# Kernel tuning notes

Measured on AMD Instinct MI355X. Metric: run time of the kernel, lower is better.

## Reference

```python
import jax, jax.numpy as jnp
import numpy as np

EPS = 1e-3        # Memory.eps distance threshold
MOMENTUM = 0.999  # Memory.momentum
N, F, M = 500000, 256, 1024


def setup_inputs() -> dict:
    key = jax.random.key(0)
    k1, k2, k3, k4, k5 = jax.random.split(key, 5)
    return {
        "points": jax.random.normal(k1, (M, 3), dtype=jnp.float32),
        "descriptors": jax.random.normal(k2, (M, F), dtype=jnp.float32),
        # learned/stateful memory bank (params/buffers of the module)
        "mem_points": jax.random.normal(k3, (N, 3), dtype=jnp.float32),
        "mem_descriptors": jax.random.normal(k4, (N, F), dtype=jnp.float32),
        "usage": jax.random.randint(k5, (N,), 0, 1000, dtype=jnp.int32),
    }


def _moving(x, m):
    # faithful to Memory.moving: x*m + (1-m)*x  (== x, kept as written)
    return x * m + (1.0 - m) * x


def reference(points, descriptors, mem_points, mem_descriptors, usage):
    # ---- point_address: cdist (p=2) + argmin nearest neighbor ----
    # squared-distance expansion; [M, N] matrix
    d2 = (jnp.sum(points * points, axis=-1)[:, None]
          + jnp.sum(mem_points * mem_points, axis=-1)[None, :]
          - 2.0 * points @ mem_points.T)
    dist = jnp.sqrt(jnp.maximum(d2, 1e-12))
    dmin = jnp.min(dist, axis=-1)
    idx = jnp.argmin(dist, axis=-1)            # [M]
    mask = dmin > EPS                          # queries with no near match

    # ---- topk eviction: lowest-usage slots, assigned in query order ----
    # torch: idx[mask] = usage.topk(k=mask.sum(), largest=False).indices
    # static-shape equivalent: take top-M least-used, select first cumsum(mask)
    _, evict = jax.lax.top_k(-usage, points.shape[0])  # [M] least-used slots
    rank = jnp.cumsum(mask.astype(jnp.int32)) - 1      # position among masked
    idx = jnp.where(mask, evict[rank], idx)

    momentum = jnp.where(mask, 0.0, MOMENTUM)[:, None]  # [M, 1]

    # ---- write: usage bump + momentum scatter-update ----
    usage_new = usage.at[idx].add(1)
    pts_new = mem_points.at[idx].set(_moving(mem_points[idx], momentum))
    desc_new = mem_descriptors.at[idx].set(_moving(mem_descriptors[idx], momentum))

    out = jnp.concatenate([pts_new, desc_new], axis=1)  # [N, 3+F]
    return out, usage_new, idx
```

## Files before the change

### kernel.cpp

```cpp
#include <hip/hip_runtime.h>

#define N_TOT   500000
#define M_Q     1024
#define QB      16
#define NSPLIT  16
#define CAND_MAX 8192

#define ARGMIN_BLKS 1024
#define HIST_BLKS   32
#define USAGE_BLKS  64
#define CROWS       16
#define COPY_BLKS   (N_TOT / CROWS)
#define MEGA_BLKS   (ARGMIN_BLKS + HIST_BLKS + USAGE_BLKS + COPY_BLKS)
#define HIST_CHUNK  (N_TOT / HIST_BLKS)

static const unsigned OUT_ROWS  = 259u * (unsigned)N_TOT;
static const unsigned OUT_USAGE = OUT_ROWS;
static const unsigned OUT_IDX   = OUT_ROWS + (unsigned)N_TOT;

#define WS_PARTKEY 0
#define WS_PARTIDX 65536
#define WS_HISTP   131072

__global__ __launch_bounds__(256) void k_mega(
    const float* __restrict__ pts,  const float* __restrict__ mpts,
    const float* __restrict__ mdesc, const int* __restrict__ usage,
    float* __restrict__ out,
    float* __restrict__ partKey, int* __restrict__ partIdx,
    int* __restrict__ histPart)
{
    __shared__ int smem[1024];
    const int b   = blockIdx.x;
    const int tid = threadIdx.x;

    if (b < ARGMIN_BLKS) {
        const int qb = b & 63;
        const int ns = b >> 6;
        const int qbase = qb * QB;
        const int chunk = N_TOT / NSPLIT;
        const int n0 = ns * chunk;
        const int n1 = n0 + chunk;

        float* qs = (float*)smem;
        float* wk = (float*)smem + 64;
        int*   wi = smem + 192;
        if (tid < QB * 3) qs[tid] = pts[qbase * 3 + tid];
        __syncthreads();

        float qx[QB], qy[QB], qz[QB];
#pragma unroll
        for (int i = 0; i < QB; i++) { qx[i] = qs[3*i]; qy[i] = qs[3*i+1]; qz[i] = qs[3*i+2]; }

        float bk[QB]; int bi[QB];
#pragma unroll
        for (int i = 0; i < QB; i++) { bk[i] = INFINITY; bi[i] = 0x7fffffff; }

        for (int n = n0 + tid; n < n1; n += 256) {
            float x = mpts[3*n+0], y = mpts[3*n+1], z = mpts[3*n+2];
            float h = 0.5f * (x*x + y*y + z*z);
#pragma unroll
            for (int i = 0; i < QB; i++) {
                float key = h - x*qx[i] - y*qy[i] - z*qz[i];
                bool lt = key < bk[i];
                bk[i] = lt ? key : bk[i];
                bi[i] = lt ? n   : bi[i];
            }
        }

        const int lane = tid & 63;
        const int wv   = tid >> 6;
#pragma unroll
        for (int off = 32; off > 0; off >>= 1) {
#pragma unroll
            for (int i = 0; i < QB; i++) {
                float ok = __shfl_down(bk[i], off, 64);
                int   oi = __shfl_down(bi[i], off, 64);
                if (ok < bk[i] || (ok == bk[i] && oi < bi[i])) { bk[i] = ok; bi[i] = oi; }
            }
        }
        if (lane == 0) {
#pragma unroll
            for (int i = 0; i < QB; i++) { wk[wv*QB + i] = bk[i]; wi[wv*QB + i] = bi[i]; }
        }
        __syncthreads();
        if (tid < QB) {
            float k = wk[tid]; int ix = wi[tid];
#pragma unroll
            for (int w = 1; w < 4; w++) {
                float ok = wk[w*QB + tid]; int oi = wi[w*QB + tid];
                if (ok < k || (ok == k && oi < ix)) { k = ok; ix = oi; }
            }
            partKey[(qbase + tid) * NSPLIT + ns] = k;
            partIdx[(qbase + tid) * NSPLIT + ns] = ix;
        }
    } else if (b < ARGMIN_BLKS + HIST_BLKS) {
        const int hb = b - ARGMIN_BLKS;
        const int r0 = hb * HIST_CHUNK;
        const int r1 = r0 + HIST_CHUNK;
#pragma unroll
        for (int i = 0; i < 4; i++) smem[tid + i * 256] = 0;
        __syncthreads();
        for (int n = r0 + tid; n < r1; n += 256) {
            unsigned v = (unsigned)usage[n];
            if (v > 1023u) v = 1023u;
            atomicAdd(&smem[v], 1);
        }
        __syncthreads();
#pragma unroll
        for (int i = 0; i < 4; i++) {
            int bin = tid + i * 256;
            histPart[hb * 1024 + bin] = smem[bin];
        }
    } else if (b < ARGMIN_BLKS + HIST_BLKS + USAGE_BLKS) {
        const int ub = b - ARGMIN_BLKS - HIST_BLKS;
        const int4* u4 = (const int4*)usage;
        float4* o4 = (float4*)(out + OUT_USAGE);
        const int TOT4 = N_TOT / 4;
        for (int g = ub * 256 + tid; g < TOT4; g += USAGE_BLKS * 256) {
            int4 u = u4[g];
            o4[g] = make_float4((float)u.x, (float)u.y, (float)u.z, (float)u.w);
        }
    } else {
        const int cb = b - (ARGMIN_BLKS + HIST_BLKS + USAGE_BLKS);
        const int n0 = cb * CROWS;
        const float4* src = (const float4*)(mdesc + (size_t)n0 * 256);
        float* obase = out + (size_t)n0 * 259;
#pragma unroll
        for (int it = 0; it < 4; it++) {
            int g = tid + it * 256;
            float4 v = src[g];
            int r = g >> 6;
            int c = (g & 63) << 2;
            *reinterpret_cast<float4*>(obase + r * 259 + 3 + c) = v;
        }
        if (tid < CROWS * 3) {
            int r = tid / 3, c = tid - r * 3;
            obase[r * 259 + c] = mpts[(size_t)n0 * 3 + tid];
        }
    }
}

__global__ __launch_bounds__(1024) void k_final(
    const float* __restrict__ pts, const int* __restrict__ usage,
    const float* __restrict__ partKey, const int* __restrict__ partIdx,
    const int* __restrict__ histPart, float* __restrict__ out)
{
    __shared__ int      scan[1024];
    __shared__ unsigned keys[CAND_MAX];
    __shared__ int      s_cnt, s_V;
    const int t = threadIdx.x;

    float bk = INFINITY; int bi = 0x7fffffff;
#pragma unroll
    for (int s = 0; s < NSPLIT; s++) {
        float k = partKey[t * NSPLIT + s];
        int   i = partIdx[t * NSPLIT + s];
        if (k < bk) { bk = k; bi = i; }
    }
    float px = pts[3*t], py = pts[3*t+1], pz = pts[3*t+2];
    float d2 = px*px + py*py + pz*pz + 2.0f * bk;
    const bool mask = d2 > 1e-6f;

    int h = 0;
#pragma unroll
    for (int b = 0; b < HIST_BLKS; b++) h += histPart[b * 1024 + t];
    scan[t] = h;
    if (t == 0) s_cnt = 0;
    __syncthreads();
    for (int off = 1; off < 1024; off <<= 1) {
        int add = (t >= off) ? scan[t - off] : 0;
        __syncthreads();
        scan[t] += add;
        __syncthreads();
    }
    int cum  = scan[t] - h;
    int cumN = scan[t];
    if (cum < M_Q && cumN >= M_Q) s_V = t;
    __syncthreads();
    const int V = s_V;

    const int4* u4 = (const int4*)usage;
    const int TOT4 = N_TOT / 4;
    for (int g = t; g < TOT4; g += 1024) {
        int4 u = u4[g];
        int n = g * 4;
#pragma unroll
        for (int j = 0; j < 4; j++) {
            int uv = (j == 0) ? u.x : (j == 1) ? u.y : (j == 2) ? u.z : u.w;
            if (uv <= V) {
                int p = atomicAdd(&s_cnt, 1);
                if (p < CAND_MAX) keys[p] = ((unsigned)uv << 19) | (unsigned)(n + j);
            }
        }
    }
    __syncthreads();
    int C = s_cnt; if (C > CAND_MAX) C = CAND_MAX;
    int P2 = 1; while (P2 < C) P2 <<= 1;
    for (int p = C + t; p < P2; p += 1024) keys[p] = 0xFFFFFFFFu;
    __syncthreads();

    for (int k = 2; k <= P2; k <<= 1) {
        for (int j = k >> 1; j > 0; j >>= 1) {
            for (int i = t; i < P2; i += 1024) {
                int ixj = i ^ j;
                if (ixj > i) {
                    unsigned a = keys[i], bb = keys[ixj];
                    bool up = ((i & k) == 0);
                    if ((a > bb) == up) { keys[i] = bb; keys[ixj] = a; }
                }
            }
            __syncthreads();
        }
    }

    scan[t] = mask ? 1 : 0; __syncthreads();
    for (int off = 1; off < 1024; off <<= 1) {
        int add = (t >= off) ? scan[t - off] : 0;
        __syncthreads();
        scan[t] += add;
        __syncthreads();
    }
    int rank = scan[t] - 1;
    int idx = mask ? (int)(keys[rank] & 0x7FFFFu) : bi;
    out[(size_t)OUT_IDX + (size_t)t] = (float)idx;
    atomicAdd(out + OUT_USAGE + idx, 1.0f);
}

extern "C" void kernel_launch(void* const* d_in, const int* in_sizes, int n_in,
                              void* d_out, int out_size, void* d_ws, size_t ws_size,
                              hipStream_t stream)
{
    (void)in_sizes; (void)n_in; (void)out_size; (void)ws_size;
    const float* pts   = (const float*)d_in[0];
    const float* mpts  = (const float*)d_in[2];
    const float* mdesc = (const float*)d_in[3];
    const int*   usage = (const int*)d_in[4];
    float* out = (float*)d_out;

    char* ws = (char*)d_ws;
    float* partKey  = (float*)(ws + WS_PARTKEY);
    int*   partIdx  = (int*)(ws + WS_PARTIDX);
    int*   histPart = (int*)(ws + WS_HISTP);

    k_mega<<<MEGA_BLKS, 256, 0, stream>>>(pts, mpts, mdesc, usage, out,
                                          partKey, partIdx, histPart);
    k_final<<<1, 1024, 0, stream>>>(pts, usage, partKey, partIdx, histPart, out);
}
```

Before: 386.9 us.

## Fuse final selection into mega kernel via global flag spin-waits

```diff
diff --git a/kernel.cpp b/kernel.cpp
--- a/kernel.cpp
+++ b/kernel.cpp
@@ -4,15 +4,25 @@
 #define M_Q     1024
 #define QB      16
 #define NSPLIT  16
-#define CAND_MAX 8192
-
+#define CAND_MAX 4096
+
+#define CROWS       16
+#define NTILES      (N_TOT / CROWS)
 #define ARGMIN_BLKS 1024
 #define HIST_BLKS   32
 #define USAGE_BLKS  64
-#define CROWS       16
-#define COPY_BLKS   (N_TOT / CROWS)
-#define MEGA_BLKS   (ARGMIN_BLKS + HIST_BLKS + USAGE_BLKS + COPY_BLKS)
+#define COLL_BLKS   64
 #define HIST_CHUNK  (N_TOT / HIST_BLKS)
+
+#define B_HIST0     ARGMIN_BLKS
+#define B_USAGE0    (B_HIST0 + HIST_BLKS)
+#define B_SCANV     (B_USAGE0 + USAGE_BLKS)
+#define B_COLL0     (B_SCANV + 1)
+#define B_FINAL     (B_COLL0 + COLL_BLKS)
+#define B_COPY0     (B_FINAL + 1)
+#define TOTAL_BLKS  (B_COPY0 + NTILES)
+
+#define TILE_F      (CROWS * 259)
 
 static const unsigned OUT_ROWS  = 259u * (unsigned)N_TOT;
 static const unsigned OUT_USAGE = OUT_ROWS;
@@ -21,19 +31,68 @@
 #define WS_PARTKEY 0
 #define WS_PARTIDX 65536
 #define WS_HISTP   131072
-
-__global__ __launch_bounds__(256) void k_mega(
+#define WS_V       262144
+#define WS_CNT     262148
+#define WS_FLAGS   262176
+#define WS_KEYS    262208
+
+#define F_HIST 0
+#define F_SCN  1
+#define F_COL  2
+#define F_ARG  3
+#define F_USG  4
+
+__device__ __forceinline__ void spin_until(int* f, int want) {
+    while (atomicAdd(f, 0) < want) __builtin_amdgcn_s_sleep(16);
+    __threadfence();
+}
+
+__global__ void k_init(int* flags, int* cnt) {
+    if (threadIdx.x < 8) flags[threadIdx.x] = 0;
+    if (threadIdx.x == 8) *cnt = 0;
+}
+
+__global__ __launch_bounds__(256, 6) void k_one(
     const float* __restrict__ pts,  const float* __restrict__ mpts,
     const float* __restrict__ mdesc, const int* __restrict__ usage,
     float* __restrict__ out,
     float* __restrict__ partKey, int* __restrict__ partIdx,
-    int* __restrict__ histPart)
+    int* __restrict__ histPart, int* __restrict__ Vp, int* __restrict__ cnt,
+    int* __restrict__ flags, unsigned* __restrict__ keysG)
 {
-    __shared__ int smem[1024];
+    __shared__ int smem[4432];
     const int b   = blockIdx.x;
     const int tid = threadIdx.x;
 
-    if (b < ARGMIN_BLKS) {
+    if (b >= B_COPY0) {
+        const int cb = b - B_COPY0;
+        const int n0 = cb * CROWS;
+        float* L = (float*)smem;
+
+        const float4* src = (const float4*)(mdesc + (size_t)n0 * 256);
+#pragma unroll
+        for (int it = 0; it < 4; it++) {
+            int g = tid + it * 256;
+            float4 v = src[g];
+            int r = g >> 6;
+            int c = (g & 63) << 2;
+            float* d = L + r * 259 + 3 + c;
+            d[0] = v.x; d[1] = v.y; d[2] = v.z; d[3] = v.w;
+        }
+        if (tid < CROWS * 3) {
+            int r = tid / 3, c = tid - r * 3;
+            L[r * 259 + c] = mpts[(size_t)n0 * 3 + tid];
+        }
+        __syncthreads();
+
+        float4* dst4 = (float4*)(out + (size_t)cb * TILE_F);
+        const float4* s4 = (const float4*)L;
+#pragma unroll
+        for (int it = 0; it < 5; it++) {
+            int g = tid + it * 256;
+            if (g < TILE_F / 4) dst4[g] = s4[g];
+        }
+    } else if (b < ARGMIN_BLKS) {
         const int qb = b & 63;
         const int ns = b >> 6;
         const int qbase = qb * QB;
@@ -93,8 +152,11 @@
             partKey[(qbase + tid) * NSPLIT + ns] = k;
             partIdx[(qbase + tid) * NSPLIT + ns] = ix;
         }
-    } else if (b < ARGMIN_BLKS + HIST_BLKS) {
-        const int hb = b - ARGMIN_BLKS;
+        __threadfence();
+        __syncthreads();
+        if (tid == 0) atomicAdd(&flags[F_ARG], 1);
+    } else if (b < B_USAGE0) {
+        const int hb = b - B_HIST0;
         const int r0 = hb * HIST_CHUNK;
         const int r1 = r0 + HIST_CHUNK;
 #pragma unroll
@@ -111,8 +173,11 @@
             int bin = tid + i * 256;
             histPart[hb * 1024 + bin] = smem[bin];
         }
-    } else if (b < ARGMIN_BLKS + HIST_BLKS + USAGE_BLKS) {
-        const int ub = b - ARGMIN_BLKS - HIST_BLKS;
+        __threadfence();
+        __syncthreads();
+        if (tid == 0) atomicAdd(&flags[F_HIST], 1);
+    } else if (b < B_SCANV) {
+        const int ub = b - B_USAGE0;
         const int4* u4 = (const int4*)usage;
         float4* o4 = (float4*)(out + OUT_USAGE);
         const int TOT4 = N_TOT / 4;
@@ -120,110 +185,121 @@
             int4 u = u4[g];
             o4[g] = make_float4((float)u.x, (float)u.y, (float)u.z, (float)u.w);
         }
+        __threadfence();
+        __syncthreads();
+        if (tid == 0) atomicAdd(&flags[F_USG], 1);
+    } else if (b == B_SCANV) {
+        if (tid == 0) spin_until(&flags[F_HIST], HIST_BLKS);
+        __syncthreads();
+        int h[4];
+#pragma unroll
+        for (int j = 0; j < 4; j++) {
+            h[j] = 0;
+            for (int bb = 0; bb < HIST_BLKS; bb++) h[j] += histPart[bb * 1024 + tid * 4 + j];
+        }
+        int lsum = h[0] + h[1] + h[2] + h[3];
+        smem[tid] = lsum; __syncthreads();
+        for (int off = 1; off < 256; off <<= 1) {
+            int add = (tid >= off) ? smem[tid - off] : 0;
+            __syncthreads();
+            smem[tid] += add;
+            __syncthreads();
+        }
+        int run = smem[tid] - lsum;
+#pragma unroll
+        for (int j = 0; j < 4; j++) {
+            int incl = run + h[j];
+            if (run < M_Q && incl >= M_Q) {
+                atomicExch(Vp, tid * 4 + j);
+                __threadfence();
+            }
+            run = incl;
+        }
+        __syncthreads();
+        if (tid == 0) atomicAdd(&flags[F_SCN], 1);
+    } else if (b < B_FINAL) {
+        const int rb = b - B_COLL0;
+        if (tid == 0) {
+            spin_until(&flags[F_SCN], 1);
+            smem[0] = atomicAdd(Vp, 0);
+        }
+        __syncthreads();
+        const int V = smem[0];
+        for (int n = rb * 256 + tid; n < N_TOT; n += COLL_BLKS * 256) {
+            int u = usage[n];
+            if (u <= V) {
+                int p = atomicAdd(cnt, 1);
+                if (p < CAND_MAX) keysG[p] = ((unsigned)u << 19) | (unsigned)n;
+            }
+        }
+        __threadfence();
+        __syncthreads();
+        if (tid == 0) atomicAdd(&flags[F_COL], 1);
     } else {
-        const int cb = b - (ARGMIN_BLKS + HIST_BLKS + USAGE_BLKS);
-        const int n0 = cb * CROWS;
-        const float4* src = (const float4*)(mdesc + (size_t)n0 * 256);
-        float* obase = out + (size_t)n0 * 259;
-#pragma unroll
-        for (int it = 0; it < 4; it++) {
-            int g = tid + it * 256;
-            float4 v = src[g];
-            int r = g >> 6;
-            int c = (g & 63) << 2;
-            *reinterpret_cast<float4*>(obase + r * 259 + 3 + c) = v;
-        }
-        if (tid < CROWS * 3) {
-            int r = tid / 3, c = tid - r * 3;
-            obase[r * 259 + c] = mpts[(size_t)n0 * 3 + tid];
+        unsigned* keys = (unsigned*)smem;
+        int* sc     = smem + 4096;
+        int* s_misc = smem + 4400;
+        if (tid == 0) {
+            spin_until(&flags[F_ARG], ARGMIN_BLKS);
+            spin_until(&flags[F_USG], USAGE_BLKS);
+            spin_until(&flags[F_COL], COLL_BLKS);
+            s_misc[0] = atomicAdd(cnt, 0);
+        }
+        __syncthreads();
+        int C = s_misc[0]; if (C > CAND_MAX) C = CAND_MAX;
+        int P2 = 1; while (P2 < C) P2 <<= 1;
+
+        int   bi4[4], msk[4];
+#pragma unroll
+        for (int j = 0; j < 4; j++) {
+            int q = tid * 4 + j;
+            float bk = INFINITY; int ix = 0x7fffffff;
+            for (int s = 0; s < NSPLIT; s++) {
+                float k = partKey[q * NSPLIT + s];
+                int   i = partIdx[q * NSPLIT + s];
+                if (k < bk) { bk = k; ix = i; }
+            }
+            float px = pts[3*q], py = pts[3*q+1], pz = pts[3*q+2];
+            float d2 = px*px + py*py + pz*pz + 2.0f * bk;
+            msk[j] = (d2 > 1e-6f) ? 1 : 0;
+            bi4[j] = ix;
+        }
+
+        for (int p = tid; p < P2; p += 256) keys[p] = (p < C) ? keysG[p] : 0xFFFFFFFFu;
+        __syncthreads();
+
+        for (int k2 = 2; k2 <= P2; k2 <<= 1) {
+            for (int j = k2 >> 1; j > 0; j >>= 1) {
+                for (int i = tid; i < P2; i += 256) {
+                    int ixj = i ^ j;
+                    if (ixj > i) {
+                        unsigned a = keys[i], bb2 = keys[ixj];
+                        bool up = ((i & k2) == 0);
+                        if ((a > bb2) == up) { keys[i] = bb2; keys[ixj] = a; }
+                    }
+                }
+                __syncthreads();
+            }
+        }
+
+        int lsum = msk[0] + msk[1] + msk[2] + msk[3];
+        sc[tid] = lsum; __syncthreads();
+        for (int off = 1; off < 256; off <<= 1) {
+            int add = (tid >= off) ? sc[tid - off] : 0;
+            __syncthreads();
+            sc[tid] += add;
+            __syncthreads();
+        }
+        int run = sc[tid] - lsum;
+#pragma unroll
+        for (int j = 0; j < 4; j++) {
+            int q = tid * 4 + j;
+            run += msk[j];
+            int idx = msk[j] ? (int)(keys[run - 1] & 0x7FFFFu) : bi4[j];
+            out[(size_t)OUT_IDX + (size_t)q] = (float)idx;
+            atomicAdd(out + OUT_USAGE + idx, 1.0f);
         }
     }
-}
-
-__global__ __launch_bounds__(1024) void k_final(
-    const float* __restrict__ pts, const int* __restrict__ usage,
-    const float* __restrict__ partKey, const int* __restrict__ partIdx,
-    const int* __restrict__ histPart, float* __restrict__ out)
-{
-    __shared__ int      scan[1024];
-    __shared__ unsigned keys[CAND_MAX];
-    __shared__ int      s_cnt, s_V;
-    const int t = threadIdx.x;
-
-    float bk = INFINITY; int bi = 0x7fffffff;
-#pragma unroll
-    for (int s = 0; s < NSPLIT; s++) {
-        float k = partKey[t * NSPLIT + s];
-        int   i = partIdx[t * NSPLIT + s];
-        if (k < bk) { bk = k; bi = i; }
-    }
-    float px = pts[3*t], py = pts[3*t+1], pz = pts[3*t+2];
-    float d2 = px*px + py*py + pz*pz + 2.0f * bk;
-    const bool mask = d2 > 1e-6f;
-
-    int h = 0;
-#pragma unroll
-    for (int b = 0; b < HIST_BLKS; b++) h += histPart[b * 1024 + t];
-    scan[t] = h;
-    if (t == 0) s_cnt = 0;
-    __syncthreads();
-    for (int off = 1; off < 1024; off <<= 1) {
-        int add = (t >= off) ? scan[t - off] : 0;
-        __syncthreads();
-        scan[t] += add;
-        __syncthreads();
-    }
-    int cum  = scan[t] - h;
-    int cumN = scan[t];
-    if (cum < M_Q && cumN >= M_Q) s_V = t;
-    __syncthreads();
-    const int V = s_V;
-
-    const int4* u4 = (const int4*)usage;
-    const int TOT4 = N_TOT / 4;
-    for (int g = t; g < TOT4; g += 1024) {
-        int4 u = u4[g];
-        int n = g * 4;
-#pragma unroll
-        for (int j = 0; j < 4; j++) {
-            int uv = (j == 0) ? u.x : (j == 1) ? u.y : (j == 2) ? u.z : u.w;
-            if (uv <= V) {
-                int p = atomicAdd(&s_cnt, 1);
-                if (p < CAND_MAX) keys[p] = ((unsigned)uv << 19) | (unsigned)(n + j);
-            }
-        }
-    }
-    __syncthreads();
-    int C = s_cnt; if (C > CAND_MAX) C = CAND_MAX;
-    int P2 = 1; while (P2 < C) P2 <<= 1;
-    for (int p = C + t; p < P2; p += 1024) keys[p] = 0xFFFFFFFFu;
-    __syncthreads();
-
-    for (int k = 2; k <= P2; k <<= 1) {
-        for (int j = k >> 1; j > 0; j >>= 1) {
-            for (int i = t; i < P2; i += 1024) {
-                int ixj = i ^ j;
-                if (ixj > i) {
-                    unsigned a = keys[i], bb = keys[ixj];
-                    bool up = ((i & k) == 0);
-                    if ((a > bb) == up) { keys[i] = bb; keys[ixj] = a; }
-                }
-            }
-            __syncthreads();
-        }
-    }
-
-    scan[t] = mask ? 1 : 0; __syncthreads();
-    for (int off = 1; off < 1024; off <<= 1) {
-        int add = (t >= off) ? scan[t - off] : 0;
-        __syncthreads();
-        scan[t] += add;
-        __syncthreads();
-    }
-    int rank = scan[t] - 1;
-    int idx = mask ? (int)(keys[rank] & 0x7FFFFu) : bi;
-    out[(size_t)OUT_IDX + (size_t)t] = (float)idx;
-    atomicAdd(out + OUT_USAGE + idx, 1.0f);
 }
 
 extern "C" void kernel_launch(void* const* d_in, const int* in_sizes, int n_in,
@@ -238,11 +314,16 @@
     float* out = (float*)d_out;
 
     char* ws = (char*)d_ws;
-    float* partKey  = (float*)(ws + WS_PARTKEY);
-    int*   partIdx  = (int*)(ws + WS_PARTIDX);
-    int*   histPart = (int*)(ws + WS_HISTP);
-
-    k_mega<<<MEGA_BLKS, 256, 0, stream>>>(pts, mpts, mdesc, usage, out,
-                                          partKey, partIdx, histPart);
-    k_final<<<1, 1024, 0, stream>>>(pts, usage, partKey, partIdx, histPart, out);
+    float*    partKey  = (float*)(ws + WS_PARTKEY);
+    int*      partIdx  = (int*)(ws + WS_PARTIDX);
+    int*      histPart = (int*)(ws + WS_HISTP);
+    int*      Vp       = (int*)(ws + WS_V);
+    int*      cnt      = (int*)(ws + WS_CNT);
+    int*      flags    = (int*)(ws + WS_FLAGS);
+    unsigned* keysG    = (unsigned*)(ws + WS_KEYS);
+
+    k_init<<<1, 64, 0, stream>>>(flags, cnt);
+    k_one<<<TOTAL_BLKS, 256, 0, stream>>>(pts, mpts, mdesc, usage, out,
+                                          partKey, partIdx, histPart,
+                                          Vp, cnt, flags, keysG);
 }
```

Measured after the change: 513.2 us. +32.6%, slower.
